# Performance work log

Hardware: AMD Instinct MI355X
Metric: run time of the kernel (lower is better)

## Reference

```python
import jax, jax.numpy as jnp
import numpy as np

B, N, D = 2, 8192, 64          # batch, points, feature dim (dim_in == dim_out)
FILTER_SIZE = 11               # k nearest neighbors in feature space
N_ITER = 5                     # mean-field iterations


def setup_inputs() -> dict:
    key = jax.random.key(0)
    k0, k1, k2, k3 = jax.random.split(key, 4)
    return {
        "logits": jax.random.normal(k0, (B, N), jnp.float32),
        "p": jax.random.normal(k1, (B, D, N), jnp.float32),
        "W1": jax.random.normal(k2, (D, D), jnp.float32) / np.float32(np.sqrt(D)),
        "b1": jnp.zeros((D,), jnp.float32),
        "W2": jax.random.normal(k3, (D, D), jnp.float32) / np.float32(np.sqrt(D)),
        "b2": jnp.zeros((D,), jnp.float32),
    }


def reference(logits, p, W1, b1, W2, b2):
    # crf_encoder: two stacked Linear layers applied to p.permute(0,2,1) -> [B,N,D]
    f = jnp.einsum('bdn,de->bne', p, W1) + b1
    f = jnp.einsum('bne,ef->bnf', f, W2) + b2  # [B,N,D] feature embedding

    # pairwise squared distances in feature space: [B,N,N]
    sq = jnp.sum(f * f, axis=-1)
    d2 = sq[:, :, None] + sq[:, None, :] - 2.0 * jnp.einsum('bnd,bmd->bnm', f, f)

    # filter_size nearest neighbors (includes self) with Gaussian weights exp(-d2)
    neg_d2, idx = jax.lax.top_k(-d2, FILTER_SIZE)   # [B,N,K]
    w = jnp.exp(neg_d2)                             # [B,N,K]

    gather = jax.vmap(lambda qb, ib: qb[ib])        # per-batch gather: [N],[N,K]->[N,K]

    # mean-field iterations (binary CRF: sigmoid marginals, unary = logits)
    u = logits
    for _ in range(N_ITER):
        q = jax.nn.sigmoid(u)                       # current marginals [B,N]
        msg = jnp.sum(w * gather(q, idx), axis=-1)  # filtered message   [B,N]
        u = logits - msg                            # compatibility transform + unary

    return jax.nn.sigmoid(u)  # return_log_proba=False -> probabilities, [B,N]
```

## Files before the change

kernel.cpp:

```cpp
#include <hip/hip_runtime.h>

#define NPTS 8192
#define NTOT 16384
#define KNB 11
#define CAP 16
#define MARG 9.0f
#define MAXM 8192

typedef __attribute__((ext_vector_type(8))) short short8;
typedef __attribute__((ext_vector_type(4))) float f32x4;

__device__ __forceinline__ unsigned short f2bf(float x) {
  union { float f; unsigned u; } v; v.f = x;
  unsigned r = v.u + 0x7FFFu + ((v.u >> 16) & 1u);
  return (unsigned short)(r >> 16);
}

__device__ __forceinline__ float sigm(float x) { return 1.f / (1.f + expf(-x)); }

__global__ __launch_bounds__(256) void k0_w12(
    const float* __restrict__ W1, const float* __restrict__ b1,
    const float* __restrict__ W2, const float* __restrict__ b2,
    float* __restrict__ W12, float* __restrict__ b12,
    unsigned* __restrict__ cnt) {
  int t = blockIdx.x * 256 + threadIdx.x;
  cnt[t] = 0u;
  if (t >= 4096) return;
  int d = t >> 6, e = t & 63;
  float s = 0.f;
  for (int kk = 0; kk < 64; ++kk) s = fmaf(W1[d * 64 + kk], W2[kk * 64 + e], s);
  W12[t] = s;
  if (d == 0) {
    float sb = b2[e];
    for (int kk = 0; kk < 64; ++kk) sb = fmaf(b1[kk], W2[kk * 64 + e], sb);
    b12[e] = sb;
  }
}

__global__ __launch_bounds__(256) void k1_encode(
    const float* __restrict__ p,
    const float* __restrict__ W12,
    const float* __restrict__ b12,
    float* __restrict__ f32f,
    unsigned short* __restrict__ fpre,
    float* __restrict__ sq,
    float* __restrict__ sq32) {
  __shared__ float sp[64 * 64];
  __shared__ float sPart[4][64];
  int t = threadIdx.x, lane = t & 63;
  int w = __builtin_amdgcn_readfirstlane(t >> 6);
  int e0 = w * 16;
  int base = blockIdx.x * 64;
  int b = base >> 13, n0 = base & (NPTS - 1);
  const float* pb = p + (size_t)b * 64 * NPTS + n0;

  int row = t >> 4, chunk = t & 15;
#pragma unroll
  for (int k = 0; k < 4; ++k) {
    int r = k * 16 + row;
    uint4 v = *(const uint4*)(pb + (size_t)r * NPTS + chunk * 4);
    *(uint4*)(sp + r * 64 + chunk * 4) = v;
  }
  __syncthreads();

  float f[16];
#pragma unroll
  for (int j = 0; j < 16; ++j) f[j] = b12[e0 + j];

#pragma unroll 8
  for (int d = 0; d < 64; ++d) {
    float pd = sp[d * 64 + lane];
#pragma unroll
    for (int j = 0; j < 16; ++j)
      f[j] = fmaf(pd, W12[d * 64 + e0 + j], f[j]);
  }

  float s = 0.f;
#pragma unroll
  for (int j = 0; j < 16; ++j) s = fmaf(f[j], f[j], s);
  sPart[w][lane] = s;
  __syncthreads();
  if (w == 0) {
    float s32 = sPart[0][lane] + sPart[1][lane];
    float s64 = s32 + (sPart[2][lane] + sPart[3][lane]);
    sq32[base + lane] = s32;
    sq[base + lane] = s64;
  }

  f32x4* o4 = (f32x4*)(f32f + (size_t)(base + lane) * 64 + e0);
#pragma unroll
  for (int jj = 0; jj < 4; ++jj) {
    f32x4 v; v[0] = f[4 * jj]; v[1] = f[4 * jj + 1]; v[2] = f[4 * jj + 2]; v[3] = f[4 * jj + 3];
    o4[jj] = v;
  }
  if (w < 2) {
    unsigned* ob = (unsigned*)(fpre + (size_t)(base + lane) * 32 + e0);
#pragma unroll
    for (int jj = 0; jj < 8; ++jj) {
      unsigned lo = f2bf(f[2 * jj]);
      unsigned hi = f2bf(f[2 * jj + 1]);
      ob[jj] = lo | (hi << 16);
    }
  }
}

__global__ __launch_bounds__(256) void k2_gram_select(
    const unsigned short* __restrict__ fpre,
    const float* __restrict__ sq32,
    unsigned* __restrict__ cnt,
    unsigned* __restrict__ cand) {
  __shared__ uint4 sB[1024];
  int bid = blockIdx.x;
  int b = (bid >= 528) ? 1 : 0;
  int rem = bid - b * 528;
  int band = (int)((sqrtf(8.f * (float)rem + 1.f) - 1.f) * 0.5f);
  if (((band + 1) * (band + 2)) / 2 <= rem) band++;
  else if ((band * (band + 1)) / 2 > rem) band--;
  int seg = rem - (band * (band + 1)) / 2;

  int t = threadIdx.x;
  int lane = t & 63;
  int arow = lane & 15;
  int q = lane >> 4;
  int wave = t >> 6;
  int rowbase = band * 256 + wave * 64;
  int cbase = seg * 256;
  const unsigned short* fb = fpre + (size_t)b * NPTS * 32;
  const float* s32b = sq32 + b * NPTS;

  const uint4* gsrc = (const uint4*)fb + (size_t)seg * 1024;
  uint4 v[4];
#pragma unroll
  for (int k = 0; k < 4; ++k) v[k] = gsrc[t + k * 256];

  short8 afrag[4];
#pragma unroll
  for (int tr = 0; tr < 4; ++tr)
    afrag[tr] = *(const short8*)(fb + (size_t)(rowbase + tr * 16 + arow) * 32 + q * 8);

  f32x4 srq[4], hh[4];
#pragma unroll
  for (int tr = 0; tr < 4; ++tr) {
    srq[tr] = *(const f32x4*)(s32b + rowbase + tr * 16 + (q << 2));
    hh[tr] = 0.5f * srq[tr];
  }
  float thrc[16];
#pragma unroll
  for (int cc = 0; cc < 4; ++cc)
#pragma unroll
    for (int tc = 0; tc < 4; ++tc)
      thrc[cc * 4 + tc] = 0.5f * s32b[cbase + cc * 64 + tc * 16 + arow] - 0.5f * MARG;

#pragma unroll
  for (int k = 0; k < 4; ++k) {
    int c = t + k * 256;
    int r = c >> 2, qq = c & 3;
    sB[r * 4 + (qq ^ (r & 3))] = v[k];
  }
  __syncthreads();

  f32x4 z4 = {0.f, 0.f, 0.f, 0.f};
  unsigned hitmask = 0u;
#pragma unroll
  for (int cc = 0; cc < 4; ++cc)
#pragma unroll
    for (int tc = 0; tc < 4; ++tc) {
      int e = cc * 4 + tc;
      int rl = cc * 64 + tc * 16 + arow;
      short8 bf = *(const short8*)&sB[rl * 4 + (q ^ (rl & 3))];
      f32x4 a0 = __builtin_amdgcn_mfma_f32_16x16x32_bf16(afrag[0], bf, z4, 0, 0, 0);
      f32x4 a1 = __builtin_amdgcn_mfma_f32_16x16x32_bf16(afrag[1], bf, z4, 0, 0, 0);
      f32x4 a2 = __builtin_amdgcn_mfma_f32_16x16x32_bf16(afrag[2], bf, z4, 0, 0, 0);
      f32x4 a3 = __builtin_amdgcn_mfma_f32_16x16x32_bf16(afrag[3], bf, z4, 0, 0, 0);
      float m0 = fmaxf(fmaxf(a0[0] - hh[0][0], a0[1] - hh[0][1]),
                       fmaxf(a0[2] - hh[0][2], a0[3] - hh[0][3]));
      float m1 = fmaxf(fmaxf(a1[0] - hh[1][0], a1[1] - hh[1][1]),
                       fmaxf(a1[2] - hh[1][2], a1[3] - hh[1][3]));
      float m2 = fmaxf(fmaxf(a2[0] - hh[2][0], a2[1] - hh[2][1]),
                       fmaxf(a2[2] - hh[2][2], a2[3] - hh[2][3]));
      float m3 = fmaxf(fmaxf(a3[0] - hh[3][0], a3[1] - hh[3][1]),
                       fmaxf(a3[2] - hh[3][2], a3[3] - hh[3][3]));
      float m = fmaxf(fmaxf(m0, m1), fmaxf(m2, m3));
      if (__ballot(m > thrc[e])) hitmask |= (1u << e);
    }

  if (hitmask) {
#pragma unroll 1
    for (int e = 0; e < 16; ++e) {
      if (!(hitmask & (1u << e))) continue;
      int cc = e >> 2, tc = e & 3;
      int rl = cc * 64 + tc * 16 + arow;
      short8 bf = *(const short8*)&sB[rl * 4 + (q ^ (rl & 3))];
      int colpt = cbase + cc * 64 + tc * 16 + arow;
      float scv = s32b[colpt];
      f32x4 acc[4];
#pragma unroll
      for (int tr = 0; tr < 4; ++tr)
        acc[tr] = __builtin_amdgcn_mfma_f32_16x16x32_bf16(afrag[tr], bf, z4, 0, 0, 0);
#pragma unroll
      for (int tr = 0; tr < 4; ++tr)
#pragma unroll
        for (int rg = 0; rg < 4; ++rg) {
          float d2 = srq[tr][rg] + scv - 2.f * acc[tr][rg];
          if (d2 < MARG) {
            int rowpt = rowbase + tr * 16 + (q << 2) + rg;
            int gr = b * NPTS + rowpt;
            union { float f; unsigned u; } cv; cv.f = d2 + 16.f;
            unsigned kb = cv.u & 0xFFFFE000u;
            unsigned slot = atomicAdd(&cnt[gr], 1u);
            if (slot < CAP) cand[gr * CAP + slot] = kb | (unsigned)colpt;
            if (band != seg) {
              int gc = b * NPTS + colpt;
              unsigned slot2 = atomicAdd(&cnt[gc], 1u);
              if (slot2 < CAP) cand[gc * CAP + slot2] = kb | (unsigned)rowpt;
            }
          }
        }
    }
  }
}

__global__ __launch_bounds__(256) void kt_self(
    const float* __restrict__ logits, const unsigned* __restrict__ cnt,
    float* __restrict__ out) {
  int i = blockIdx.x * 256 + threadIdx.x;
  if (cnt[i] > 1u) return;
  float lg = logits[i];
  float u = lg;
#pragma unroll
  for (int it = 0; it < 5; ++it) u = lg - sigm(u);
  out[i] = sigm(u);
}

__global__ __launch_bounds__(512) void kt_multi(
    const float* __restrict__ f32f, const float* __restrict__ sq,
    const unsigned* __restrict__ cnt, const unsigned* __restrict__ cand,
    float* __restrict__ Wbuf, int* __restrict__ IDXb,
    const float* __restrict__ logits, float* __restrict__ out) {
  __shared__ float qs[NTOT];
  __shared__ int slist[MAXM];
  __shared__ float su[MAXM];
  __shared__ int sctr;
  int t = threadIdx.x;
  if (t == 0) sctr = 0;
  __syncthreads();

#pragma unroll 1
  for (int j = 0; j < 32; ++j) {
    int i = j * 512 + t;
    if (cnt[i] > 1u) {
      qs[i] = sigm(logits[i]);
      int slot = atomicAdd(&sctr, 1);
      if (slot < MAXM) slist[slot] = i;
    }
  }
  __syncthreads();
  int nm = sctr; if (nm > MAXM) nm = MAXM;

#pragma unroll 1
  for (int k = t; k < nm; k += 512) {
    int r = slist[k];
    int bb = r >> 13;
    unsigned count = cnt[r]; if (count > CAP) count = CAP;
    unsigned kky[CAP];
#pragma unroll
    for (int jj = 0; jj < CAP; ++jj)
      kky[jj] = (jj < (int)count) ? cand[r * CAP + jj] : 0xFFFFFFFFu;
#pragma unroll
    for (int a = 0; a < CAP - 1; ++a)
#pragma unroll
      for (int cc = 0; cc < CAP - 1; ++cc) {
        unsigned lo = min(kky[cc], kky[cc + 1]);
        unsigned hi = max(kky[cc], kky[cc + 1]);
        kky[cc] = lo; kky[cc + 1] = hi;
      }
    float fr[64];
    const f32x4* fr4 = (const f32x4*)(f32f + (size_t)r * 64);
#pragma unroll
    for (int jj = 0; jj < 16; ++jj) {
      f32x4 v = fr4[jj];
      fr[4 * jj] = v[0]; fr[4 * jj + 1] = v[1]; fr[4 * jj + 2] = v[2]; fr[4 * jj + 3] = v[3];
    }
    float sqr = sq[r];
    int nsel = (int)count < KNB ? (int)count : KNB;
#pragma unroll 1
    for (int kk = 0; kk < KNB; ++kk) {
      float w = 0.f;
      int gi = r;
      if (kk < nsel) {
        int col = (int)(kky[kk] & 8191u);
        gi = bb * NPTS + col;
        const float* fm = f32f + (size_t)gi * 64;
        float dot = 0.f;
#pragma unroll
        for (int d = 0; d < 64; ++d) dot = fmaf(fr[d], fm[d], dot);
        float d2 = sqr + sq[gi] - 2.f * dot;
        w = expf(-d2);
      }
      Wbuf[(size_t)r * KNB + kk] = w;
      IDXb[(size_t)r * KNB + kk] = gi;
    }
  }
  __threadfence();
  __syncthreads();

  for (int it = 0; it < 5; ++it) {
#pragma unroll 1
    for (int k = t; k < nm; k += 512) {
      int r = slist[k];
      float msg = 0.f;
      const float* wp = Wbuf + (size_t)r * KNB;
      const int* ip = IDXb + (size_t)r * KNB;
#pragma unroll
      for (int kk = 0; kk < KNB; ++kk) msg = fmaf(wp[kk], qs[ip[kk]], msg);
      su[k] = logits[r] - msg;
    }
    __syncthreads();
#pragma unroll 1
    for (int k = t; k < nm; k += 512) qs[slist[k]] = sigm(su[k]);
    __syncthreads();
  }
#pragma unroll 1
  for (int k = t; k < nm; k += 512) out[slist[k]] = sigm(su[k]);
}

extern "C" void kernel_launch(void* const* d_in, const int* in_sizes, int n_in,
                              void* d_out, int out_size, void* d_ws, size_t ws_size,
                              hipStream_t stream) {
  const float* logits = (const float*)d_in[0];
  const float* p      = (const float*)d_in[1];
  const float* W1     = (const float*)d_in[2];
  const float* b1     = (const float*)d_in[3];
  const float* W2     = (const float*)d_in[4];
  const float* b2     = (const float*)d_in[5];
  float* out = (float*)d_out;

  char* ws = (char*)d_ws;
  float* W12 = (float*)ws;
  float* b12 = W12 + 4096;
  float* f32f = b12 + 64;
  unsigned short* fpre = (unsigned short*)(f32f + (size_t)NTOT * 64);
  float* sq = (float*)(fpre + (size_t)NTOT * 32);
  float* sq32 = sq + NTOT;
  unsigned* cnt = (unsigned*)(sq32 + NTOT);
  unsigned* cand = cnt + NTOT;
  float* Wbuf = (float*)(cand + (size_t)NTOT * CAP);
  int* IDX = (int*)(Wbuf + (size_t)NTOT * KNB);

  k0_w12<<<64, 256, 0, stream>>>(W1, b1, W2, b2, W12, b12, cnt);
  k1_encode<<<256, 256, 0, stream>>>(p, W12, b12, f32f, fpre, sq, sq32);
  k2_gram_select<<<1056, 256, 0, stream>>>(fpre, sq32, cnt, cand);
  kt_self<<<64, 256, 0, stream>>>(logits, cnt, out);
  kt_multi<<<1, 512, 0, stream>>>(f32f, sq, cnt, cand, Wbuf, IDX, logits, out);
}
```

Before: 125.0 us.

## Move neighbor weight computation out of single-block kernel into grid-wide kernel

Neighbor sorting, exact distance recomputation and Gaussian weight evaluation for multi-candidate points previously ran inside a single 512-thread block. That work now runs in a 64-block kernel merged with the self-only path, one thread per point. The single-block mean-field iteration kernel is widened to 1024 threads and only reads the precomputed weights and indices. This removes a serial bottleneck in which one CU did all the 64-dim dot products, at the cost of keeping one single-block kernel for the iterations.

```diff
diff --git a/kernel.cpp b/kernel.cpp
--- a/kernel.cpp
+++ b/kernel.cpp
@@ -220,22 +220,68 @@
   }
 }
 
-__global__ __launch_bounds__(256) void kt_self(
-    const float* __restrict__ logits, const unsigned* __restrict__ cnt,
-    float* __restrict__ out) {
-  int i = blockIdx.x * 256 + threadIdx.x;
-  if (cnt[i] > 1u) return;
-  float lg = logits[i];
-  float u = lg;
-#pragma unroll
-  for (int it = 0; it < 5; ++it) u = lg - sigm(u);
-  out[i] = sigm(u);
-}
-
-__global__ __launch_bounds__(512) void kt_multi(
+__global__ __launch_bounds__(256) void k3_fused(
     const float* __restrict__ f32f, const float* __restrict__ sq,
     const unsigned* __restrict__ cnt, const unsigned* __restrict__ cand,
     float* __restrict__ Wbuf, int* __restrict__ IDXb,
+    const float* __restrict__ logits, float* __restrict__ out) {
+  int r = blockIdx.x * 256 + threadIdx.x;
+  int b = r >> 13;
+  unsigned count = cnt[r];
+  if (count <= 1u) {
+    float lg = logits[r];
+    float u = lg;
+#pragma unroll
+    for (int it = 0; it < 5; ++it) u = lg - sigm(u);
+    out[r] = sigm(u);
+    return;
+  }
+  if (count > CAP) count = CAP;
+
+  unsigned k[CAP];
+#pragma unroll
+  for (int j = 0; j < CAP; ++j)
+    k[j] = (j < (int)count) ? cand[r * CAP + j] : 0xFFFFFFFFu;
+#pragma unroll
+  for (int a = 0; a < CAP - 1; ++a)
+#pragma unroll
+    for (int c = 0; c < CAP - 1; ++c) {
+      unsigned lo = min(k[c], k[c + 1]);
+      unsigned hi = max(k[c], k[c + 1]);
+      k[c] = lo; k[c + 1] = hi;
+    }
+
+  float fr[64];
+  const f32x4* fr4 = (const f32x4*)(f32f + (size_t)r * 64);
+#pragma unroll
+  for (int j = 0; j < 16; ++j) {
+    f32x4 v = fr4[j];
+    fr[4 * j] = v[0]; fr[4 * j + 1] = v[1]; fr[4 * j + 2] = v[2]; fr[4 * j + 3] = v[3];
+  }
+  float sqr = sq[r];
+  int nsel = (int)count < KNB ? (int)count : KNB;
+#pragma unroll
+  for (int kk = 0; kk < KNB; ++kk) {
+    float w = 0.f;
+    int gi = r;
+    if (kk < nsel) {
+      int col = (int)(k[kk] & 8191u);
+      gi = b * NPTS + col;
+      const float* fm = f32f + (size_t)gi * 64;
+      float dot = 0.f;
+#pragma unroll
+      for (int d = 0; d < 64; ++d) dot = fmaf(fr[d], fm[d], dot);
+      float d2 = sqr + sq[gi] - 2.f * dot;
+      w = expf(-d2);
+    }
+    Wbuf[(size_t)r * KNB + kk] = w;
+    IDXb[(size_t)r * KNB + kk] = gi;
+  }
+}
+
+__global__ __launch_bounds__(1024) void kt_iter(
+    const unsigned* __restrict__ cnt,
+    const float* __restrict__ Wbuf, const int* __restrict__ IDXb,
     const float* __restrict__ logits, float* __restrict__ out) {
   __shared__ float qs[NTOT];
   __shared__ int slist[MAXM];
@@ -246,8 +292,8 @@
   __syncthreads();
 
 #pragma unroll 1
-  for (int j = 0; j < 32; ++j) {
-    int i = j * 512 + t;
+  for (int j = 0; j < 16; ++j) {
+    int i = j * 1024 + t;
     if (cnt[i] > 1u) {
       qs[i] = sigm(logits[i]);
       int slot = atomicAdd(&sctr, 1);
@@ -257,56 +303,9 @@
   __syncthreads();
   int nm = sctr; if (nm > MAXM) nm = MAXM;
 
-#pragma unroll 1
-  for (int k = t; k < nm; k += 512) {
-    int r = slist[k];
-    int bb = r >> 13;
-    unsigned count = cnt[r]; if (count > CAP) count = CAP;
-    unsigned kky[CAP];
-#pragma unroll
-    for (int jj = 0; jj < CAP; ++jj)
-      kky[jj] = (jj < (int)count) ? cand[r * CAP + jj] : 0xFFFFFFFFu;
-#pragma unroll
-    for (int a = 0; a < CAP - 1; ++a)
-#pragma unroll
-      for (int cc = 0; cc < CAP - 1; ++cc) {
-        unsigned lo = min(kky[cc], kky[cc + 1]);
-        unsigned hi = max(kky[cc], kky[cc + 1]);
-        kky[cc] = lo; kky[cc + 1] = hi;
-      }
-    float fr[64];
-    const f32x4* fr4 = (const f32x4*)(f32f + (size_t)r * 64);
-#pragma unroll
-    for (int jj = 0; jj < 16; ++jj) {
-      f32x4 v = fr4[jj];
-      fr[4 * jj] = v[0]; fr[4 * jj + 1] = v[1]; fr[4 * jj + 2] = v[2]; fr[4 * jj + 3] = v[3];
-    }
-    float sqr = sq[r];
-    int nsel = (int)count < KNB ? (int)count : KNB;
-#pragma unroll 1
-    for (int kk = 0; kk < KNB; ++kk) {
-      float w = 0.f;
-      int gi = r;
-      if (kk < nsel) {
-        int col = (int)(kky[kk] & 8191u);
-        gi = bb * NPTS + col;
-        const float* fm = f32f + (size_t)gi * 64;
-        float dot = 0.f;
-#pragma unroll
-        for (int d = 0; d < 64; ++d) dot = fmaf(fr[d], fm[d], dot);
-        float d2 = sqr + sq[gi] - 2.f * dot;
-        w = expf(-d2);
-      }
-      Wbuf[(size_t)r * KNB + kk] = w;
-      IDXb[(size_t)r * KNB + kk] = gi;
-    }
-  }
-  __threadfence();
-  __syncthreads();
-
   for (int it = 0; it < 5; ++it) {
 #pragma unroll 1
-    for (int k = t; k < nm; k += 512) {
+    for (int k = t; k < nm; k += 1024) {
       int r = slist[k];
       float msg = 0.f;
       const float* wp = Wbuf + (size_t)r * KNB;
@@ -317,11 +316,11 @@
     }
     __syncthreads();
 #pragma unroll 1
-    for (int k = t; k < nm; k += 512) qs[slist[k]] = sigm(su[k]);
+    for (int k = t; k < nm; k += 1024) qs[slist[k]] = sigm(su[k]);
     __syncthreads();
   }
 #pragma unroll 1
-  for (int k = t; k < nm; k += 512) out[slist[k]] = sigm(su[k]);
+  for (int k = t; k < nm; k += 1024) out[slist[k]] = sigm(su[k]);
 }
 
 extern "C" void kernel_launch(void* const* d_in, const int* in_sizes, int n_in,
@@ -350,6 +349,6 @@
   k0_w12<<<64, 256, 0, stream>>>(W1, b1, W2, b2, W12, b12, cnt);
   k1_encode<<<256, 256, 0, stream>>>(p, W12, b12, f32f, fpre, sq, sq32);
   k2_gram_select<<<1056, 256, 0, stream>>>(fpre, sq32, cnt, cand);
-  kt_self<<<64, 256, 0, stream>>>(logits, cnt, out);
-  kt_multi<<<1, 512, 0, stream>>>(f32f, sq, cnt, cand, Wbuf, IDX, logits, out);
-}
+  k3_fused<<<64, 256, 0, stream>>>(f32f, sq, cnt, cand, Wbuf, IDX, logits, out);
+  kt_iter<<<1, 1024, 0, stream>>>(cnt, Wbuf, IDX, logits, out);
+}
```

Result: faster. 116.0 us (-7.2%).
